# Kernel optimization log

Measured on AMD Instinct MI355X. Metric: run time of the kernel, lower is better.

Reference implementation:

```python
import jax, jax.numpy as jnp
import numpy as np

N, E, IN, H, OUT = 50000, 600000, 256, 128, 40
EPS, GAMMA = 0.1, 0.1  # PyG AntiSymmetricConv defaults


def _build_norm(edge_index, n):
    # GCNConv normalization with added self loops: D^-1/2 (A+I) D^-1/2
    loops = jnp.arange(n, dtype=edge_index.dtype)
    src = jnp.concatenate([edge_index[0], loops])
    dst = jnp.concatenate([edge_index[1], loops])
    deg = jax.ops.segment_sum(jnp.ones(src.shape[0], dtype=jnp.float32), dst, num_segments=n)
    dinv = jnp.where(deg > 0, jax.lax.rsqrt(jnp.maximum(deg, 1e-12)), 0.0)
    return src, dst, dinv[src] * dinv[dst]


def _gcn(x, w, src, dst, norm, n):
    # GCNConv(bias=False): scatter normalized messages to target nodes
    m = (x @ w)[src] * norm[:, None]          # [E+N, d]
    return jax.ops.segment_sum(m, dst, num_segments=n)


def _antisym_conv(x, W, gcn_w, bias, src, dst, norm, num_iters):
    d = W.shape[0]
    aW = W - W.T - GAMMA * jnp.eye(d, dtype=W.dtype)  # antisymmetric weight
    n = x.shape[0]

    def step(h, _):
        upd = jnp.tanh(h @ aW.T + _gcn(h, gcn_w, src, dst, norm, n) + bias)
        return h + EPS * upd, None

    x, _ = jax.lax.scan(step, x, None, length=num_iters)
    return x


def setup_inputs() -> dict:
    key = jax.random.key(0)
    ks = jax.random.split(key, 16)
    s = lambda fan: 1.0 / np.sqrt(fan)
    return {
        "x": jax.random.normal(ks[0], (N, IN), dtype=jnp.float32),
        "edge_index": jax.random.randint(ks[1], (2, E), 0, N, dtype=jnp.int64),
        "w_hid": jax.random.normal(ks[2], (H, IN), dtype=jnp.float32) * s(IN),
        "b_hid": jax.random.normal(ks[3], (H,), dtype=jnp.float32) * s(IN),
        "W_a1": jax.random.normal(ks[4], (H, H), dtype=jnp.float32) * s(H),
        "gcn_w1": jax.random.normal(ks[5], (H, H), dtype=jnp.float32) * s(H),
        "b_a1": jax.random.normal(ks[6], (H,), dtype=jnp.float32) * s(H),
        "w_hid2": jax.random.normal(ks[7], (H // 2, H), dtype=jnp.float32) * s(H),
        "b_hid2": jax.random.normal(ks[8], (H // 2,), dtype=jnp.float32) * s(H),
        "W_a2": jax.random.normal(ks[9], (H // 2, H // 2), dtype=jnp.float32) * s(H // 2),
        "gcn_w2": jax.random.normal(ks[10], (H // 2, H // 2), dtype=jnp.float32) * s(H // 2),
        "b_a2": jax.random.normal(ks[11], (H // 2,), dtype=jnp.float32) * s(H // 2),
        "w_fc": jax.random.normal(ks[12], (OUT, H // 2), dtype=jnp.float32) * s(H // 2),
        "b_fc": jax.random.normal(ks[13], (OUT,), dtype=jnp.float32) * s(H // 2),
    }


def reference(x, edge_index, w_hid, b_hid, W_a1, gcn_w1, b_a1,
              w_hid2, b_hid2, W_a2, gcn_w2, b_a2, w_fc, b_fc):
    n = x.shape[0]
    src, dst, norm = _build_norm(edge_index, n)
    h = jax.nn.leaky_relu(x @ w_hid.T + b_hid)          # dropout is no-op in eval
    h = _antisym_conv(h, W_a1, gcn_w1, b_a1, src, dst, norm, num_iters=3)
    h = jax.nn.leaky_relu(h)
    h = jax.nn.leaky_relu(h @ w_hid2.T + b_hid2)
    h = _antisym_conv(h, W_a2, gcn_w2, b_a2, src, dst, norm, num_iters=1)
    out = h @ w_fc.T + b_fc
    return jax.nn.log_softmax(out, axis=1)
```

## Files before the change

kernel.cpp:

```cpp
#include <hip/hip_runtime.h>
#include <hip/hip_bf16.h>
#include <math.h>

typedef unsigned short u16;
typedef unsigned int   u32;
using short8  = __attribute__((ext_vector_type(8))) short;
using f32x4   = __attribute__((ext_vector_type(4))) float;

static constexpr int NNODE = 50000;
static constexpr int NEDGE = 600000;
static constexpr float EPSC   = 0.1f;
static constexpr float GAMMAC = 0.1f;

static constexpr int NTILE = (NNODE + 63) / 64;
static constexpr int XDEG  = 242;

static constexpr long long O_DINV   = 0;
static constexpr long long O_DEGI   = 50000;
static constexpr long long O_ROWPTR = 100000;
static constexpr long long O_CURSOR = 150004;
static constexpr long long O_GCUR   = 200052;
static constexpr long long O_ECSR   = 200260;
static constexpr long long O_WHB    = 1400260;
static constexpr long long O_G1TB   = O_WHB  + 16384;
static constexpr long long O_AW1B   = O_G1TB + 8192;
static constexpr long long O_W2B    = O_AW1B + 8192;
static constexpr long long O_AW2B   = O_W2B  + 4096;
static constexpr long long O_G2TB   = O_AW2B + 2048;
static constexpr long long O_WFCB   = O_G2TB + 2048;
static constexpr long long O_AGGB   = 3450004;
static constexpr long long O_HB0    = O_AGGB + 3200000;
static constexpr long long O_HB1    = O_HB0  + 3200000;
static constexpr long long O_S0     = O_HB1  + 3200000;
static constexpr long long O_S1     = O_S0   + 1600000;

__device__ __forceinline__ float bf2f(u16 u) {
    return __uint_as_float(((unsigned)u) << 16);
}
__device__ __forceinline__ u16 f2bf(float f) {
    unsigned u = __float_as_uint(f);
    return (u16)((u + 0x7FFFu + ((u >> 16) & 1u)) >> 16);
}
__device__ __forceinline__ float ftanh(float x) {
    float x2 = fminf(fmaxf(2.f * x, -30.f), 30.f);
    float e = __expf(x2);
    return (e - 1.f) * __builtin_amdgcn_rcpf(e + 1.f);
}
__device__ __forceinline__ u16 pk_fp8(float a, float b) {
    int pk = __builtin_amdgcn_cvt_pk_fp8_f32(a, b, 0, false);
    return (u16)(pk & 0xffff);
}
__device__ __forceinline__ void acc_fp8x4(float* a, u32 v, float w) {
    a[0] += __builtin_amdgcn_cvt_f32_fp8(v, 0) * w;
    a[1] += __builtin_amdgcn_cvt_f32_fp8(v, 1) * w;
    a[2] += __builtin_amdgcn_cvt_f32_fp8(v, 2) * w;
    a[3] += __builtin_amdgcn_cvt_f32_fp8(v, 3) * w;
}

__global__ __launch_bounds__(256) void prep_kernel(
    const float* __restrict__ w_hid, const float* __restrict__ W_a1,
    const float* __restrict__ gcn1,  const float* __restrict__ w2,
    const float* __restrict__ W_a2,  const float* __restrict__ gcn2,
    const float* __restrict__ wfc,   float* __restrict__ ws)
{
    int j = blockIdx.x * 256 + threadIdx.x;
    if (j < 32768) { ((u16*)(ws+O_WHB))[j] = f2bf(w_hid[j]); return; } j -= 32768;
    if (j < 16384) { int r=j>>7, c=j&127; ((u16*)(ws+O_G1TB))[j] = f2bf(gcn1[c*128+r]); return; } j -= 16384;
    if (j < 16384) { int r=j>>7, c=j&127;
                     ((u16*)(ws+O_AW1B))[j] = f2bf(W_a1[r*128+c] - W_a1[c*128+r] - (r==c?GAMMAC:0.f));
                     return; } j -= 16384;
    if (j < 8192)  { ((u16*)(ws+O_W2B))[j] = f2bf(w2[j]); return; } j -= 8192;
    if (j < 4096)  { int r=j>>6, c=j&63;
                     ((u16*)(ws+O_AW2B))[j] = f2bf(W_a2[r*64+c] - W_a2[c*64+r] - (r==c?GAMMAC:0.f));
                     return; } j -= 4096;
    if (j < 4096)  { int r=j>>6, c=j&63; ((u16*)(ws+O_G2TB))[j] = f2bf(gcn2[c*64+r]); return; } j -= 4096;
    if (j < 2560)  { ((u16*)(ws+O_WFCB))[j] = f2bf(wfc[j]); return; } j -= 2560;
    if (j < NNODE) { ((int*)(ws+O_DEGI))[j] = 0; return; } j -= NNODE;
    if (j == 0)    { ((int*)(ws+O_GCUR))[0] = 0; }
}

__global__ __launch_bounds__(256) void alloc_kernel(const int* __restrict__ degi,
                                                    float* __restrict__ dinv,
                                                    int* __restrict__ rowptr,
                                                    int* __restrict__ cursor,
                                                    int* __restrict__ gcur) {
    int i = blockIdx.x * 256 + threadIdx.x;
    if (i >= NNODE) return;
    int d = degi[i];
    dinv[i] = rsqrtf(1.0f + (float)d);
    int pos = atomicAdd(gcur, d);
    rowptr[i] = pos;
    cursor[i] = pos;
}
__global__ __launch_bounds__(256) void fill_kernel(const int* __restrict__ ei,
                                                   const float* __restrict__ dinv,
                                                   int* __restrict__ cursor,
                                                   int2* __restrict__ ecsr) {
    int e = blockIdx.x * 256 + threadIdx.x;
    if (e >= NEDGE) return;
    int s = ei[e], d = ei[NEDGE + e];
    int pos = atomicAdd(&cursor[d], 1);
    int2 v;
    v.x = s;
    v.y = __float_as_int(dinv[s] * dinv[d]);
    ecsr[pos] = v;
}

template<int KS, int NT, int AF32, int LOADACT, int EPI>
__global__ __launch_bounds__(256, 4) void mgemm(
    const void* __restrict__ Araw,
    const u16* __restrict__ Bt,
    const float* __restrict__ bias,
    float* __restrict__ outF,
    u16* __restrict__ outB,
    u16* __restrict__ outB8,
    int M, int Nn, int ldc,
    const int* __restrict__ ei,
    int* __restrict__ degi)
{
    if (ei && blockIdx.x >= NTILE) {
        for (int e = (blockIdx.x - NTILE) * 256 + threadIdx.x; e < NEDGE; e += XDEG * 256)
            atomicAdd(&degi[ei[NEDGE + e]], 1);
        return;
    }

    constexpr int K    = KS * 32;
    constexpr int KCHU = (K > 128) ? 128 : K;
    constexpr int KC   = KCHU / 32;
    constexpr int NCH  = K / KCHU;
    constexpr int P    = KCHU + 8;
    constexpr int ROWS = NT * 16;
    constexpr int CW   = NT * 16 + 1;
    constexpr int BSZ  = ROWS * P * 2;
    constexpr int ASZ  = 64 * CW * 4;
    constexpr int SMEM = BSZ > ASZ ? BSZ : ASZ;
    __shared__ __align__(16) char smem[SMEM];
    u16*   bl   = (u16*)smem;
    float* accL = (float*)smem;

    const int wave = threadIdx.x >> 6;
    const int lane = threadIdx.x & 63;
    const int m = lane & 15, q = lane >> 4;
    const int rowbase = blockIdx.x * 64 + wave * 16;
    const int row = rowbase + m;
    const bool rok = row < M;
    const short8 z8 = {0,0,0,0,0,0,0,0};

    short8 af[KS];
    if (AF32) {
        const float* apf = (const float*)Araw + (long long)row * K;
        #pragma unroll
        for (int k = 0; k < KS; ++k) {
            short8 t = z8;
            if (rok) {
                const float4* p = (const float4*)(apf + (k * 4 + q) * 8);
                float4 a = p[0], b = p[1];
                t[0]=(short)f2bf(a.x); t[1]=(short)f2bf(a.y); t[2]=(short)f2bf(a.z); t[3]=(short)f2bf(a.w);
                t[4]=(short)f2bf(b.x); t[5]=(short)f2bf(b.y); t[6]=(short)f2bf(b.z); t[7]=(short)f2bf(b.w);
            }
            af[k] = t;
        }
    } else {
        const short8* ap = (const short8*)((const u16*)Araw + (long long)row * K);
        #pragma unroll
        for (int k = 0; k < KS; ++k) af[k] = rok ? ap[k * 4 + q] : z8;
    }
    if (LOADACT) {
        #pragma unroll
        for (int k = 0; k < KS; ++k)
            #pragma unroll
            for (int e = 0; e < 8; ++e) {
                float f = bf2f((u16)af[k][e]);
                f = f > 0.f ? f : 0.01f * f;
                af[k][e] = (short)f2bf(f);
            }
    }

    f32x4 acc[NT];
    #pragma unroll
    for (int j = 0; j < NT; ++j) acc[j] = (f32x4){0.f,0.f,0.f,0.f};

    for (int ch = 0; ch < NCH; ++ch) {
        if (ch) __syncthreads();
        constexpr int CHUNKS = ROWS * (KCHU / 8);
        for (int t = threadIdx.x; t < CHUNKS; t += 256) {
            int r = t / (KCHU / 8), c = t - r * (KCHU / 8);
            short8 v = z8;
            if (r < Nn) v = *(const short8*)&Bt[(long long)r * K + ch * KCHU + c * 8];
            *(short8*)&bl[r * P + c * 8] = v;
        }
        __syncthreads();
        #pragma unroll
        for (int j = 0; j < NT; ++j) {
            #pragma unroll
            for (int k = 0; k < KC; ++k) {
                short8 bf_ = *(const short8*)&bl[(j * 16 + m) * P + k * 32 + q * 8];
                acc[j] = __builtin_amdgcn_mfma_f32_16x16x32_bf16(af[ch * KC + k], bf_, acc[j], 0, 0, 0);
            }
        }
    }

    __syncthreads();
    #pragma unroll
    for (int j = 0; j < NT; ++j)
        #pragma unroll
        for (int r = 0; r < 4; ++r)
            accL[(wave * 16 + q * 4 + r) * CW + j * 16 + m] = acc[j][r];
    __syncthreads();

    const int c0 = lane * 2;
    if (c0 < NT * 16) {
        float2 bv = {0.f, 0.f};
        if (bias) {
            if (c0 < Nn)     bv.x = bias[c0];
            if (c0 + 1 < Nn) bv.y = bias[c0 + 1];
        }
        #pragma unroll
        for (int rl = 0; rl < 16; ++rl) {
            int rowD = rowbase + rl;
            if (rowD >= M) continue;
            float2 v = *(const float2*)&accL[(wave * 16 + rl) * CW + c0];
            long long o = (long long)rowD * ldc + c0;
            v.x += bv.x; v.y += bv.y;
            if (EPI == 1) {
                v.x = v.x > 0.f ? v.x : 0.01f * v.x;
                v.y = v.y > 0.f ? v.y : 0.01f * v.y;
            }
            if (c0 + 1 < Nn) {
                if (outB) { ushort2 ob; ob.x = f2bf(v.x); ob.y = f2bf(v.y);
                            *(ushort2*)&outB[o] = ob; }
                if (outB8) outB8[o >> 1] = pk_fp8(v.x, v.y);
                if (outF) { *(float2*)&outF[o] = v; }
            } else if (c0 < Nn) {
                if (outB) outB[o] = f2bf(v.x);
                if (outF) outF[o] = v.x;
            }
        }
    }
}

template<int HD>
__global__ __launch_bounds__(256) void gather_kernel(
    const int* __restrict__ rowptr, const int* __restrict__ degi,
    const int2* __restrict__ ecsr, const float* __restrict__ dinv,
    const u32* __restrict__ g8, u16* __restrict__ aggB)
{
    int node = (blockIdx.x * 256 + threadIdx.x) >> 6;
    int lane = threadIdx.x & 63;
    if (node >= NNODE) return;
    const int qr = lane >> 4, l4 = lane & 15;
    const int r0 = rowptr[node];
    const int r1 = r0 + degi[node];
    const float wself = dinv[node] * dinv[node];
    constexpr int EL = (HD == 128) ? 8 : 4;

    float a[EL];
    #pragma unroll
    for (int i = 0; i < EL; ++i) a[i] = 0.f;
    if (qr == 0) {
        if (HD == 128) {
            uint2 gv = ((const uint2*)g8)[(long long)node * 16 + l4];
            acc_fp8x4(a, gv.x, wself);
            acc_fp8x4(a + 4, gv.y, wself);
        } else {
            u32 gv = g8[(long long)node * 16 + l4];
            acc_fp8x4(a, gv, wself);
        }
    }

    for (int base = r0; base < r1; base += 64) {
        int idx = base + lane;
        int cs = 0; float cw = 0.f;
        if (idx < r1) { int2 ev = ecsr[idx]; cs = ev.x; cw = __int_as_float(ev.y); }
        int cnt = min(64, r1 - base);
        for (int j = 0; j < cnt; j += 16) {
            #pragma unroll
            for (int u = 0; u < 4; ++u) {
                int jj = j + u * 4 + qr;
                int   s = __shfl(cs, jj);
                float w = __shfl(cw, jj);
                if (HD == 128) {
                    uint2 gv = ((const uint2*)g8)[(long long)s * 16 + l4];
                    acc_fp8x4(a, gv.x, w);
                    acc_fp8x4(a + 4, gv.y, w);
                } else {
                    u32 gv = g8[(long long)s * 16 + l4];
                    acc_fp8x4(a, gv, w);
                }
            }
        }
    }

    #pragma unroll
    for (int i = 0; i < EL; ++i) {
        a[i] += __shfl_xor(a[i], 16);
        a[i] += __shfl_xor(a[i], 32);
    }
    if (HD == 128) {
        float v0 = (qr == 0) ? a[0] : (qr == 1) ? a[2] : (qr == 2) ? a[4] : a[6];
        float v1 = (qr == 0) ? a[1] : (qr == 1) ? a[3] : (qr == 2) ? a[5] : a[7];
        long long o = (long long)node * 128 + l4 * 8 + qr * 2;
        ushort2 ob; ob.x = f2bf(v0); ob.y = f2bf(v1);
        *(ushort2*)&aggB[o] = ob;
    } else {
        float v = (qr == 0) ? a[0] : (qr == 1) ? a[1] : (qr == 2) ? a[2] : a[3];
        aggB[(long long)node * 64 + l4 * 4 + qr] = f2bf(v);
    }
}

template<int KS, int NT, int TAIL>
__global__ __launch_bounds__(256, TAIL ? 3 : 4) void mgemm_conv(
    const u16* __restrict__ hA,
    const u16* __restrict__ gA,
    const u16* __restrict__ BtW,
    const u16* __restrict__ BtG,
    const float* __restrict__ bias,
    u16* __restrict__ outB,
    u16* __restrict__ outB8,
    const u16* __restrict__ w2W,
    const float* __restrict__ b2,
    int M)
{
    constexpr int K    = KS * 32;
    constexpr int Nn   = NT * 16;
    constexpr int P    = K + 8;
    constexpr int CW   = Nn + 1;
    constexpr int BSZ  = Nn * P * 2;
    constexpr int ASZ  = 64 * CW * 4;
    constexpr int R1   = BSZ > ASZ ? BSZ : ASZ;
    constexpr int EXTRA = TAIL ? 64 * P * 2 : 0;
    __shared__ __align__(16) char smem[R1 + EXTRA];
    u16*   bl   = (u16*)smem;
    float* accL = (float*)smem;
    u16*   aggT = (u16*)(smem + R1);

    const int wave = threadIdx.x >> 6;
    const int lane = threadIdx.x & 63;
    const int m = lane & 15, q = lane >> 4;
    const int rowbase = blockIdx.x * 64 + wave * 16;
    const int row = rowbase + m;
    const bool rok = row < M;
    const short8 z8 = {0,0,0,0,0,0,0,0};

    short8 af1[KS], af2[KS];
    {
        const short8* ap1 = (const short8*)(hA + (long long)row * K);
        const short8* ap2 = (const short8*)(gA + (long long)row * K);
        #pragma unroll
        for (int k = 0; k < KS; ++k) {
            af1[k] = rok ? ap1[k * 4 + q] : z8;
            af2[k] = rok ? ap2[k * 4 + q] : z8;
        }
    }

    f32x4 acc[NT];
    #pragma unroll
    for (int j = 0; j < NT; ++j) acc[j] = (f32x4){0.f,0.f,0.f,0.f};

    #pragma unroll
    for (int pass = 0; pass < 2; ++pass) {
        const u16* Bcur = pass ? BtG : BtW;
        if (pass) __syncthreads();
        constexpr int CHUNKS = Nn * (K / 8);
        for (int t = threadIdx.x; t < CHUNKS; t += 256) {
            int r = t / (K / 8), c = t - r * (K / 8);
            *(short8*)&bl[r * P + c * 8] = *(const short8*)&Bcur[(long long)r * K + c * 8];
        }
        __syncthreads();
        #pragma unroll
        for (int j = 0; j < NT; ++j) {
            #pragma unroll
            for (int k = 0; k < KS; ++k) {
                short8 bf_ = *(const short8*)&bl[(j * 16 + m) * P + k * 32 + q * 8];
                acc[j] = __builtin_amdgcn_mfma_f32_16x16x32_bf16(
                    pass ? af2[k] : af1[k], bf_, acc[j], 0, 0, 0);
            }
        }
    }

    __syncthreads();
    #pragma unroll
    for (int j = 0; j < NT; ++j)
        #pragma unroll
        for (int r = 0; r < 4; ++r)
            accL[(wave * 16 + q * 4 + r) * CW + j * 16 + m] = acc[j][r];
    __syncthreads();

    const int c0 = lane * 2;
    if (TAIL == 0) {
        if (c0 < Nn) {
            float2 bv = {bias[c0], bias[c0 + 1]};
            #pragma unroll
            for (int rl = 0; rl < 16; ++rl) {
                int rowD = rowbase + rl;
                if (rowD >= M) continue;
                float2 v = *(const float2*)&accL[(wave * 16 + rl) * CW + c0];
                long long o = (long long)rowD * Nn + c0;
                ushort2 hh = *(const ushort2*)&hA[o];
                float n0 = bf2f(hh.x) + EPSC * ftanh(v.x + bv.x);
                float n1 = bf2f(hh.y) + EPSC * ftanh(v.y + bv.y);
                ushort2 ob; ob.x = f2bf(n0); ob.y = f2bf(n1);
                *(ushort2*)&outB[o] = ob;
                if (outB8) outB8[o >> 1] = pk_fp8(n0, n1);
            }
        }
        return;
    }

    {
        float2 bv = {bias[c0], bias[c0 + 1]};
        #pragma unroll
        for (int rl = 0; rl < 16; ++rl) {
            int rowD = rowbase + rl;
            float n0 = 0.f, n1 = 0.f;
            if (rowD < M) {
                float2 v = *(const float2*)&accL[(wave * 16 + rl) * CW + c0];
                long long o = (long long)rowD * K + c0;
                ushort2 hh = *(const ushort2*)&hA[o];
                n0 = bf2f(hh.x) + EPSC * ftanh(v.x + bv.x);
                n1 = bf2f(hh.y) + EPSC * ftanh(v.y + bv.y);
                n0 = n0 > 0.f ? n0 : 0.01f * n0;
                n1 = n1 > 0.f ? n1 : 0.01f * n1;
            }
            ushort2 ob; ob.x = f2bf(n0); ob.y = f2bf(n1);
            *(ushort2*)&aggT[(wave * 16 + rl) * P + c0] = ob;
        }
    }
    __syncthreads();

    short8 af3[4];
    #pragma unroll
    for (int k = 0; k < 4; ++k)
        af3[k] = *(const short8*)&aggT[(wave * 16 + m) * P + k * 32 + q * 8];

    {
        constexpr int CH2 = 64 * 16;
        for (int t = threadIdx.x; t < CH2; t += 256) {
            int r = t >> 4, c = t & 15;
            *(short8*)&bl[r * P + c * 8] = *(const short8*)&w2W[(long long)r * K + c * 8];
        }
    }
    __syncthreads();

    f32x4 acc2[4];
    #pragma unroll
    for (int j = 0; j < 4; ++j) acc2[j] = (f32x4){0.f,0.f,0.f,0.f};
    #pragma unroll
    for (int j = 0; j < 4; ++j)
        #pragma unroll
        for (int k = 0; k < 4; ++k) {
            short8 bf_ = *(const short8*)&bl[(j * 16 + m) * P + k * 32 + q * 8];
            acc2[j] = __builtin_amdgcn_mfma_f32_16x16x32_bf16(af3[k], bf_, acc2[j], 0, 0, 0);
        }

    __syncthreads();
    constexpr int CW2 = 65;
    #pragma unroll
    for (int j = 0; j < 4; ++j)
        #pragma unroll
        for (int r = 0; r < 4; ++r)
            accL[(wave * 16 + q * 4 + r) * CW2 + j * 16 + m] = acc2[j][r];
    __syncthreads();

    if (c0 < 64) {
        float2 bv = {b2[c0], b2[c0 + 1]};
        #pragma unroll
        for (int rl = 0; rl < 16; ++rl) {
            int rowD = rowbase + rl;
            if (rowD >= M) continue;
            float2 v = *(const float2*)&accL[(wave * 16 + rl) * CW2 + c0];
            v.x += bv.x; v.y += bv.y;
            v.x = v.x > 0.f ? v.x : 0.01f * v.x;
            v.y = v.y > 0.f ? v.y : 0.01f * v.y;
            long long o = (long long)rowD * 64 + c0;
            ushort2 ob; ob.x = f2bf(v.x); ob.y = f2bf(v.y);
            *(ushort2*)&outB[o] = ob;
            outB8[o >> 1] = pk_fp8(v.x, v.y);
        }
    }
}

__global__ __launch_bounds__(256, 4) void conv2fc(
    const u16* __restrict__ hA,
    const u16* __restrict__ gA,
    const u16* __restrict__ BtW, const u16* __restrict__ BtG,
    const float* __restrict__ bias,
    const u16* __restrict__ wfcB, const float* __restrict__ bfc,
    float* __restrict__ outF, int M)
{
    constexpr int K  = 64, NT = 4, KS = 2;
    constexpr int P  = K + 8;
    constexpr int CW = 65;
    constexpr int R1 = 64 * CW * 4;
    __shared__ __align__(16) char smem[R1 + 64 * P * 2];
    u16*   bl   = (u16*)smem;
    float* accL = (float*)smem;
    u16*   aggT = (u16*)(smem + R1);

    const int wave = threadIdx.x >> 6;
    const int lane = threadIdx.x & 63;
    const int m = lane & 15, q = lane >> 4;
    const int rowbase = blockIdx.x * 64 + wave * 16;
    const int row = rowbase + m;
    const bool rok = row < M;
    const short8 z8 = {0,0,0,0,0,0,0,0};

    short8 af1[KS], af2[KS];
    {
        const short8* ap1 = (const short8*)(hA + (long long)row * K);
        const short8* ap2 = (const short8*)(gA + (long long)row * K);
        #pragma unroll
        for (int k = 0; k < KS; ++k) {
            af1[k] = rok ? ap1[k * 4 + q] : z8;
            af2[k] = rok ? ap2[k * 4 + q] : z8;
        }
    }

    f32x4 acc[NT];
    #pragma unroll
    for (int j = 0; j < NT; ++j) acc[j] = (f32x4){0.f,0.f,0.f,0.f};

    #pragma unroll
    for (int pass = 0; pass < 2; ++pass) {
        const u16* Bcur = pass ? BtG : BtW;
        if (pass) __syncthreads();
        constexpr int CHUNKS = 64 * (K / 8);
        for (int t = threadIdx.x; t < CHUNKS; t += 256) {
            int r = t >> 3, c = t & 7;
            *(short8*)&bl[r * P + c * 8] = *(const short8*)&Bcur[(long long)r * K + c * 8];
        }
        __syncthreads();
        #pragma unroll
        for (int j = 0; j < NT; ++j)
            #pragma unroll
            for (int k = 0; k < KS; ++k) {
                short8 bf_ = *(const short8*)&bl[(j * 16 + m) * P + k * 32 + q * 8];
                acc[j] = __builtin_amdgcn_mfma_f32_16x16x32_bf16(
                    pass ? af2[k] : af1[k], bf_, acc[j], 0, 0, 0);
            }
    }

    __syncthreads();
    #pragma unroll
    for (int j = 0; j < NT; ++j)
        #pragma unroll
        for (int r = 0; r < 4; ++r)
            accL[(wave * 16 + q * 4 + r) * CW + j * 16 + m] = acc[j][r];
    __syncthreads();

    {
        const int c0 = lane * 2;
        float2 bv = {bias[c0 & 63], bias[(c0 + 1) & 63]};
        if (c0 < 64) {
            #pragma unroll
            for (int rl = 0; rl < 16; ++rl) {
                int rowD = rowbase + rl;
                float n0 = 0.f, n1 = 0.f;
                if (rowD < M) {
                    float2 v = *(const float2*)&accL[(wave * 16 + rl) * CW + c0];
                    long long o = (long long)rowD * 64 + c0;
                    ushort2 hh = *(const ushort2*)&hA[o];
                    n0 = bf2f(hh.x) + EPSC * ftanh(v.x + bv.x);
                    n1 = bf2f(hh.y) + EPSC * ftanh(v.y + bv.y);
                }
                ushort2 ob; ob.x = f2bf(n0); ob.y = f2bf(n1);
                *(ushort2*)&aggT[(wave * 16 + rl) * P + c0] = ob;
            }
        }
    }
    __syncthreads();

    short8 af4[KS];
    #pragma unroll
    for (int k = 0; k < KS; ++k)
        af4[k] = *(const short8*)&aggT[(wave * 16 + m) * P + k * 32 + q * 8];

    {
        constexpr int CHF = 48 * 8;
        for (int t = threadIdx.x; t < CHF; t += 256) {
            int r = t >> 3, c = t & 7;
            short8 v = z8;
            if (r < 40) v = *(const short8*)&wfcB[(long long)r * K + c * 8];
            *(short8*)&bl[r * P + c * 8] = v;
        }
    }
    __syncthreads();

    f32x4 acc3[3];
    #pragma unroll
    for (int j = 0; j < 3; ++j) acc3[j] = (f32x4){0.f,0.f,0.f,0.f};
    #pragma unroll
    for (int j = 0; j < 3; ++j)
        #pragma unroll
        for (int k = 0; k < KS; ++k) {
            short8 bf_ = *(const short8*)&bl[(j * 16 + m) * P + k * 32 + q * 8];
            acc3[j] = __builtin_amdgcn_mfma_f32_16x16x32_bf16(af4[k], bf_, acc3[j], 0, 0, 0);
        }

    __syncthreads();
    constexpr int CW3 = 49;
    #pragma unroll
    for (int j = 0; j < 3; ++j)
        #pragma unroll
        for (int r = 0; r < 4; ++r)
            accL[(wave * 16 + q * 4 + r) * CW3 + j * 16 + m] = acc3[j][r];
    __syncthreads();

    float mrow = 0.f, lrow = 0.f;
    if (lane < 16) {
        const float* rp = &accL[(wave * 16 + lane) * CW3];
        float mx = -1e30f;
        for (int c = 0; c < 40; ++c) mx = fmaxf(mx, rp[c] + bfc[c]);
        float s = 0.f;
        for (int c = 0; c < 40; ++c) s += expf(rp[c] + bfc[c] - mx);
        mrow = mx; lrow = logf(s);
    }
    for (int rl = 0; rl < 16; ++rl) {
        float mm = __shfl(mrow, rl);
        float ll = __shfl(lrow, rl);
        int rowD = rowbase + rl;
        if (rowD < M && lane < 40) {
            float v = accL[(wave * 16 + rl) * CW3 + lane] + bfc[lane];
            outF[(long long)rowD * 40 + lane] = v - mm - ll;
        }
    }
}

extern "C" void kernel_launch(void* const* d_in, const int* in_sizes, int n_in,
                              void* d_out, int out_size, void* d_ws, size_t ws_size,
                              hipStream_t stream) {
    const float* x     = (const float*)d_in[0];
    const int*   ei    = (const int*)d_in[1];
    const float* w_hid = (const float*)d_in[2];
    const float* b_hid = (const float*)d_in[3];
    const float* W_a1  = (const float*)d_in[4];
    const float* gcn1  = (const float*)d_in[5];
    const float* b_a1  = (const float*)d_in[6];
    const float* w2    = (const float*)d_in[7];
    const float* b2    = (const float*)d_in[8];
    const float* W_a2  = (const float*)d_in[9];
    const float* gcn2  = (const float*)d_in[10];
    const float* b_a2  = (const float*)d_in[11];
    const float* wfc   = (const float*)d_in[12];
    const float* bfc   = (const float*)d_in[13];
    float* ws = (float*)d_ws;
    float* out = (float*)d_out;

    float* dinv   = ws + O_DINV;
    int*   degi   = (int*)(ws + O_DEGI);
    int*   rowptr = (int*)(ws + O_ROWPTR);
    int*   cursor = (int*)(ws + O_CURSOR);
    int*   gcur   = (int*)(ws + O_GCUR);
    int2*  ecsr   = (int2*)(ws + O_ECSR);
    u16* whB  = (u16*)(ws + O_WHB);
    u16* g1tB = (u16*)(ws + O_G1TB);
    u16* aw1B = (u16*)(ws + O_AW1B);
    u16* w2B  = (u16*)(ws + O_W2B);
    u16* aw2B = (u16*)(ws + O_AW2B);
    u16* g2tB = (u16*)(ws + O_G2TB);
    u16* wfcB = (u16*)(ws + O_WFCB);
    u16* aggB = (u16*)(ws + O_AGGB);
    u16* hB0  = (u16*)(ws + O_HB0);
    u16* hB1  = (u16*)(ws + O_HB1);
    u16* s0   = (u16*)(ws + O_S0);
    u16* s1   = (u16*)(ws + O_S1);

    const int nNodeB = (NNODE + 255) / 256;

    prep_kernel<<<(84480 + NNODE + 256 + 255) / 256, 256, 0, stream>>>(
        w_hid, W_a1, gcn1, w2, W_a2, gcn2, wfc, ws);

    const int gatherBlocks = (NNODE * 64 + 255) / 256;

    mgemm<8, 8, 1, 0, 1><<<NTILE + XDEG, 256, 0, stream>>>(
        x, whB, b_hid, nullptr, hB0, s0, NNODE, 128, 128, ei, degi);

    alloc_kernel<<<nNodeB, 256, 0, stream>>>(degi, dinv, rowptr, cursor, gcur);
    fill_kernel<<<(NEDGE + 255) / 256, 256, 0, stream>>>(ei, dinv, cursor, ecsr);

    gather_kernel<128><<<gatherBlocks, 256, 0, stream>>>(
        rowptr, degi, ecsr, dinv, (const u32*)s0, aggB);
    mgemm_conv<4, 8, 0><<<NTILE, 256, 0, stream>>>(
        hB0, aggB, aw1B, g1tB, b_a1, hB1, s1, nullptr, nullptr, NNODE);
    gather_kernel<128><<<gatherBlocks, 256, 0, stream>>>(
        rowptr, degi, ecsr, dinv, (const u32*)s1, aggB);
    mgemm_conv<4, 8, 0><<<NTILE, 256, 0, stream>>>(
        hB1, aggB, aw1B, g1tB, b_a1, hB0, s0, nullptr, nullptr, NNODE);
    gather_kernel<128><<<gatherBlocks, 256, 0, stream>>>(
        rowptr, degi, ecsr, dinv, (const u32*)s0, aggB);
    mgemm_conv<4, 8, 1><<<NTILE, 256, 0, stream>>>(
        hB0, aggB, aw1B, g1tB, b_a1, hB1, s1, w2B, b2, NNODE);

    gather_kernel<64><<<gatherBlocks, 256, 0, stream>>>(
        rowptr, degi, ecsr, dinv, (const u32*)s1, aggB);
    conv2fc<<<NTILE, 256, 0, stream>>>(
        hB1, aggB, aw2B, g2tB, b_a2, wfcB, bfc, out, NNODE);
}
```

Before: 362.8 us.

## Build CSR via per-block LDS histograms instead of global atomics

Replaces the global-atomic degree count and cursor-based CSR fill with a two-level scheme. 128 edge chunks each build packed 16-bit LDS histograms over four node ranges and write per-chunk partial counts. A per-node prefix over chunks then gives offsets, with a wave-level scan plus one atomic per wave for rowptr. The fill kernel re-derives ranks with LDS atomics, giving deterministic edge order and removing contended global atomics. The edge weight now stores only dinv[src], and the destination dinv factor moves into the gather epilogue. In exchange it adds 12.8 MB of partial and base arrays, four passes over edges in each block, and a fill kernel limited to 128 blocks, which may underuse the GPU.

```diff
diff --git a/kernel.cpp b/kernel.cpp
--- a/kernel.cpp
+++ b/kernel.cpp
@@ -13,13 +13,15 @@
 static constexpr float GAMMAC = 0.1f;
 
 static constexpr int NTILE = (NNODE + 63) / 64;
-static constexpr int XDEG  = 242;
+static constexpr int GH    = 128;
+static constexpr int NRNG  = 12500;
+static constexpr int NWORD = NRNG / 2;
+static constexpr int NPASS = 4;
 
 static constexpr long long O_DINV   = 0;
 static constexpr long long O_DEGI   = 50000;
 static constexpr long long O_ROWPTR = 100000;
-static constexpr long long O_CURSOR = 150004;
-static constexpr long long O_GCUR   = 200052;
+static constexpr long long O_GCUR   = 150004;
 static constexpr long long O_ECSR   = 200260;
 static constexpr long long O_WHB    = 1400260;
 static constexpr long long O_G1TB   = O_WHB  + 16384;
@@ -33,6 +35,8 @@
 static constexpr long long O_HB1    = O_HB0  + 3200000;
 static constexpr long long O_S0     = O_HB1  + 3200000;
 static constexpr long long O_S1     = O_S0   + 1600000;
+static constexpr long long O_PART   = O_S1   + 1600000;
+static constexpr long long O_BASE   = O_PART + 3200000;
 
 __device__ __forceinline__ float bf2f(u16 u) {
     return __uint_as_float(((unsigned)u) << 16);
@@ -75,35 +79,72 @@
                      return; } j -= 4096;
     if (j < 4096)  { int r=j>>6, c=j&63; ((u16*)(ws+O_G2TB))[j] = f2bf(gcn2[c*64+r]); return; } j -= 4096;
     if (j < 2560)  { ((u16*)(ws+O_WFCB))[j] = f2bf(wfc[j]); return; } j -= 2560;
-    if (j < NNODE) { ((int*)(ws+O_DEGI))[j] = 0; return; } j -= NNODE;
     if (j == 0)    { ((int*)(ws+O_GCUR))[0] = 0; }
 }
 
-__global__ __launch_bounds__(256) void alloc_kernel(const int* __restrict__ degi,
-                                                    float* __restrict__ dinv,
-                                                    int* __restrict__ rowptr,
-                                                    int* __restrict__ cursor,
-                                                    int* __restrict__ gcur) {
+__global__ __launch_bounds__(256) void alloc_kernel(
+    const u16* __restrict__ part, float* __restrict__ dinv,
+    int* __restrict__ degi, int* __restrict__ rowptr,
+    u16* __restrict__ base16, int* __restrict__ gcur)
+{
     int i = blockIdx.x * 256 + threadIdx.x;
-    if (i >= NNODE) return;
-    int d = degi[i];
-    dinv[i] = rsqrtf(1.0f + (float)d);
-    int pos = atomicAdd(gcur, d);
-    rowptr[i] = pos;
-    cursor[i] = pos;
-}
-__global__ __launch_bounds__(256) void fill_kernel(const int* __restrict__ ei,
-                                                   const float* __restrict__ dinv,
-                                                   int* __restrict__ cursor,
-                                                   int2* __restrict__ ecsr) {
-    int e = blockIdx.x * 256 + threadIdx.x;
-    if (e >= NEDGE) return;
-    int s = ei[e], d = ei[NEDGE + e];
-    int pos = atomicAdd(&cursor[d], 1);
-    int2 v;
-    v.x = s;
-    v.y = __float_as_int(dinv[s] * dinv[d]);
-    ecsr[pos] = v;
+    int lane = threadIdx.x & 63;
+    bool ok = i < NNODE;
+    int deg = 0;
+    if (ok) {
+        int run = 0;
+        #pragma unroll 4
+        for (int g = 0; g < GH; ++g) {
+            base16[(long long)g * NNODE + i] = (u16)run;
+            run += part[(long long)g * NNODE + i];
+        }
+        deg = run;
+        degi[i] = deg;
+        dinv[i] = rsqrtf(1.0f + (float)deg);
+    }
+    int run = deg;
+    #pragma unroll
+    for (int off = 1; off < 64; off <<= 1) {
+        int v = __shfl_up(run, off);
+        if (lane >= off) run += v;
+    }
+    int tot = __shfl(run, 63);
+    int basep = 0;
+    if (lane == 63) basep = atomicAdd(gcur, tot);
+    basep = __shfl(basep, 63);
+    if (ok) rowptr[i] = basep + run - deg;
+}
+
+__global__ __launch_bounds__(256) void fill_kernel(
+    const int* __restrict__ ei, const float* __restrict__ dinv,
+    const int* __restrict__ rowptr, const u16* __restrict__ base16,
+    int2* __restrict__ ecsr)
+{
+    __shared__ u32 cur[NWORD];
+    const int g = blockIdx.x;
+    const long long e0 = (long long)g * NEDGE / GH;
+    const long long e1 = (long long)(g + 1) * NEDGE / GH;
+    const u16* bb = base16 + (long long)g * NNODE;
+    for (int pass = 0; pass < NPASS; ++pass) {
+        const int nbase = pass * NRNG;
+        for (int wi = threadIdx.x; wi < NWORD; wi += 256) cur[wi] = 0;
+        __syncthreads();
+        for (long long e = e0 + threadIdx.x; e < e1; e += 256) {
+            int d = ei[NEDGE + e];
+            int r = d - nbase;
+            if ((unsigned)r < (unsigned)NRNG) {
+                int s = ei[e];
+                u32 old = atomicAdd(&cur[r >> 1], 1u << ((r & 1) * 16));
+                int rank = (int)((old >> ((r & 1) * 16)) & 0xffffu);
+                int slot = rowptr[d] + (int)bb[d] + rank;
+                int2 v;
+                v.x = s;
+                v.y = __float_as_int(dinv[s]);
+                ecsr[slot] = v;
+            }
+        }
+        __syncthreads();
+    }
 }
 
 template<int KS, int NT, int AF32, int LOADACT, int EPI>
@@ -116,14 +157,8 @@
     u16* __restrict__ outB8,
     int M, int Nn, int ldc,
     const int* __restrict__ ei,
-    int* __restrict__ degi)
+    u16* __restrict__ partial)
 {
-    if (ei && blockIdx.x >= NTILE) {
-        for (int e = (blockIdx.x - NTILE) * 256 + threadIdx.x; e < NEDGE; e += XDEG * 256)
-            atomicAdd(&degi[ei[NEDGE + e]], 1);
-        return;
-    }
-
     constexpr int K    = KS * 32;
     constexpr int KCHU = (K > 128) ? 128 : K;
     constexpr int KC   = KCHU / 32;
@@ -135,6 +170,31 @@
     constexpr int ASZ  = 64 * CW * 4;
     constexpr int SMEM = BSZ > ASZ ? BSZ : ASZ;
     __shared__ __align__(16) char smem[SMEM];
+
+    if (ei && blockIdx.x >= NTILE) {
+        int g = blockIdx.x - NTILE;
+        u32* hist = (u32*)smem;
+        const long long e0 = (long long)g * NEDGE / GH;
+        const long long e1 = (long long)(g + 1) * NEDGE / GH;
+        u16* part = partial + (long long)g * NNODE;
+        for (int pass = 0; pass < NPASS; ++pass) {
+            const int nbase = pass * NRNG;
+            for (int wi = threadIdx.x; wi < NWORD; wi += 256) hist[wi] = 0;
+            __syncthreads();
+            for (long long e = e0 + threadIdx.x; e < e1; e += 256) {
+                int d = ei[NEDGE + e];
+                int r = d - nbase;
+                if ((unsigned)r < (unsigned)NRNG)
+                    atomicAdd(&hist[r >> 1], 1u << ((r & 1) * 16));
+            }
+            __syncthreads();
+            for (int wi = threadIdx.x; wi < NWORD; wi += 256)
+                *(u32*)&part[nbase + wi * 2] = hist[wi];
+            __syncthreads();
+        }
+        return;
+    }
+
     u16*   bl   = (u16*)smem;
     float* accL = (float*)smem;
 
@@ -251,7 +311,7 @@
     const int qr = lane >> 4, l4 = lane & 15;
     const int r0 = rowptr[node];
     const int r1 = r0 + degi[node];
-    const float wself = dinv[node] * dinv[node];
+    const float dn = dinv[node];
     constexpr int EL = (HD == 128) ? 8 : 4;
 
     float a[EL];
@@ -260,11 +320,11 @@
     if (qr == 0) {
         if (HD == 128) {
             uint2 gv = ((const uint2*)g8)[(long long)node * 16 + l4];
-            acc_fp8x4(a, gv.x, wself);
-            acc_fp8x4(a + 4, gv.y, wself);
+            acc_fp8x4(a, gv.x, dn);
+            acc_fp8x4(a + 4, gv.y, dn);
         } else {
             u32 gv = g8[(long long)node * 16 + l4];
-            acc_fp8x4(a, gv, wself);
+            acc_fp8x4(a, gv, dn);
         }
     }
 
@@ -299,12 +359,13 @@
     if (HD == 128) {
         float v0 = (qr == 0) ? a[0] : (qr == 1) ? a[2] : (qr == 2) ? a[4] : a[6];
         float v1 = (qr == 0) ? a[1] : (qr == 1) ? a[3] : (qr == 2) ? a[5] : a[7];
+        v0 *= dn; v1 *= dn;
         long long o = (long long)node * 128 + l4 * 8 + qr * 2;
         ushort2 ob; ob.x = f2bf(v0); ob.y = f2bf(v1);
         *(ushort2*)&aggB[o] = ob;
     } else {
         float v = (qr == 0) ? a[0] : (qr == 1) ? a[1] : (qr == 2) ? a[2] : a[3];
-        aggB[(long long)node * 64 + l4 * 4 + qr] = f2bf(v);
+        aggB[(long long)node * 64 + l4 * 4 + qr] = f2bf(v * dn);
     }
 }
 
@@ -649,7 +710,6 @@
     float* dinv   = ws + O_DINV;
     int*   degi   = (int*)(ws + O_DEGI);
     int*   rowptr = (int*)(ws + O_ROWPTR);
-    int*   cursor = (int*)(ws + O_CURSOR);
     int*   gcur   = (int*)(ws + O_GCUR);
     int2*  ecsr   = (int2*)(ws + O_ECSR);
     u16* whB  = (u16*)(ws + O_WHB);
@@ -664,19 +724,20 @@
     u16* hB1  = (u16*)(ws + O_HB1);
     u16* s0   = (u16*)(ws + O_S0);
     u16* s1   = (u16*)(ws + O_S1);
-
-    const int nNodeB = (NNODE + 255) / 256;
-
-    prep_kernel<<<(84480 + NNODE + 256 + 255) / 256, 256, 0, stream>>>(
+    u16* part = (u16*)(ws + O_PART);
+    u16* base16 = (u16*)(ws + O_BASE);
+
+    prep_kernel<<<(84481 + 255) / 256, 256, 0, stream>>>(
         w_hid, W_a1, gcn1, w2, W_a2, gcn2, wfc, ws);
 
     const int gatherBlocks = (NNODE * 64 + 255) / 256;
 
-    mgemm<8, 8, 1, 0, 1><<<NTILE + XDEG, 256, 0, stream>>>(
-        x, whB, b_hid, nullptr, hB0, s0, NNODE, 128, 128, ei, degi);
-
-    alloc_kernel<<<nNodeB, 256, 0, stream>>>(degi, dinv, rowptr, cursor, gcur);
-    fill_kernel<<<(NEDGE + 255) / 256, 256, 0, stream>>>(ei, dinv, cursor, ecsr);
+    mgemm<8, 8, 1, 0, 1><<<NTILE + GH, 256, 0, stream>>>(
+        x, whB, b_hid, nullptr, hB0, s0, NNODE, 128, 128, ei, part);
+
+    alloc_kernel<<<(NNODE + 255) / 256, 256, 0, stream>>>(
+        part, dinv, degi, rowptr, base16, gcur);
+    fill_kernel<<<GH, 256, 0, stream>>>(ei, dinv, rowptr, base16, ecsr);
 
     gather_kernel<128><<<gatherBlocks, 256, 0, stream>>>(
         rowptr, degi, ecsr, dinv, (const u32*)s0, aggB);
```

After: 383.2 us. +5.6%, slower.
